# Kernel tuning notes

Hardware: AMD Instinct MI355X
Metric: run time of the kernel (lower is better)

## Reference

```python
import jax, jax.numpy as jnp
import numpy as np

DIS_NORM = 6.0 * 512 / 1000.0  # 6 * D(z=0) * Nmesh / Boxsize with D(0)=1


def setup_inputs() -> dict:
    key = jax.random.key(0)
    x = jax.random.normal(key, (2, 4, 128, 128, 128), dtype=jnp.float32)
    return {"x": x}


def _lag2eul(x):
    N, C = x.shape[0], x.shape[1]
    D, H, W = x.shape[2], x.shape[3], x.shape[4]
    P = D * H * W
    Cout = C - 3 if C > 3 else 1

    # rm_dis_mean=True: mean displacement, detached
    dis_mean = jax.lax.stop_gradient(jnp.mean(x[:, :3], axis=(2, 3, 4), keepdims=True))

    pos = (x[:, :3] - dis_mean) * DIS_NORM  # (N,3,D,H,W)
    gd = jnp.arange(D, dtype=x.dtype) + 0.5
    gh = jnp.arange(H, dtype=x.dtype) + 0.5
    gw = jnp.arange(W, dtype=x.dtype) + 0.5
    grid = jnp.stack(jnp.meshgrid(gd, gh, gw, indexing='ij'))  # (3,D,H,W)
    pos = (pos + grid[None]).reshape(N, 3, P)

    if C > 3:
        val = x[:, 3:].reshape(N, Cout, P)
    else:
        val = jnp.ones((N, Cout, P), dtype=x.dtype)

    intpos = jnp.floor(pos).astype(jnp.int32)
    # 8 trilinear neighbors: bit b of n -> offset along dim b
    neighbors = (jnp.arange(8, dtype=jnp.int32)[None, :] >> jnp.arange(3, dtype=jnp.int32)[:, None]) & 1  # (3,8)
    tgt = intpos[:, :, :, None] + neighbors[None, :, None, :]  # (N,3,P,8)

    kernel = jnp.prod(1.0 - jnp.abs(pos[:, :, :, None] - tgt.astype(x.dtype)), axis=1)  # (N,P,8)
    src = val[:, :, :, None] * kernel[:, None, :, :]  # (N,Cout,P,8)

    # periodic=False: mask out-of-bounds deposits
    bounds = jnp.array([D, H, W], dtype=jnp.int32)[None, :, None, None]
    mask = jnp.all((tgt >= 0) & (tgt < bounds), axis=1)  # (N,P,8)
    ind = (tgt[:, 0] * H + tgt[:, 1]) * W + tgt[:, 2]  # (N,P,8)
    ind = jnp.clip(ind, 0, P - 1)
    src = jnp.where(mask[:, None, :, :], src, jnp.zeros((), dtype=x.dtype))

    def scatter_one(ind_n, src_n):
        mesh = jnp.zeros((Cout, P), dtype=src_n.dtype)
        return mesh.at[:, ind_n.reshape(-1)].add(src_n.reshape(Cout, -1))

    mesh = jax.vmap(scatter_one)(ind, src)  # (N,Cout,P)
    return mesh.reshape(N, Cout, D, H, W)


def reference(x):
    return _lag2eul(x)
```

## Files before the change

kernel.cpp:

```cpp
#include <hip/hip_runtime.h>

#define NBATCH 2
#define NDIM   128
#define NP     (128 * 128 * 128)
#define DIS_NORM 3.072f

#define TS   16
#define LO   5
#define HI   6
#define WIN  (TS + LO + HI)
#define WIN2 (WIN * WIN)
#define WINF (WIN * WIN * WIN)
#define TPB  8
#define NTILE (TPB * TPB * TPB)
#define NTHR 512

#define FXSCALE 16777216.0f
#define FXINV   (1.0f / 16777216.0f)

#define QCAP 1280

#define SLAB 19696

#define SUMS_OFF 0
#define SLABS_OFF 1024
#define WS_FLOATS ((size_t)SLABS_OFF + (size_t)NBATCH * NTILE * SLAB)
#define WS_NEEDED_BYTES (WS_FLOATS * sizeof(float))

__device__ __constant__ int BASE27[27] = {
    0,216,792,972,1548,3084,3564,3744,4224,
    4376,4952,6488,6968,8504,12600,13880,14360,15640,
    16040,16220,16700,16852,17332,18612,19012,19164,19564};

__global__ __launch_bounds__(256) void prep_kernel(const float* __restrict__ x,
                                                   float* __restrict__ ws,
                                                   float* __restrict__ out) {
    const int plane = blockIdx.y;
    if (plane < 6) {
        const int n = plane / 3, c = plane % 3;
        const float4* xp = (const float4*)(x + ((size_t)n * 4 + c) * NP);
        float s = 0.0f;
        for (int i = blockIdx.x * 256 + threadIdx.x; i < NP / 4; i += 128 * 256) {
            float4 v = xp[i];
            s += (v.x + v.y) + (v.z + v.w);
        }
        #pragma unroll
        for (int off = 32; off > 0; off >>= 1) s += __shfl_down(s, off, 64);
        __shared__ float wsum[4];
        if ((threadIdx.x & 63) == 0) wsum[threadIdx.x >> 6] = s;
        __syncthreads();
        if (threadIdx.x == 0)
            ws[SUMS_OFF + plane * 128 + blockIdx.x] =
                (wsum[0] + wsum[1]) + (wsum[2] + wsum[3]);
    } else {
        float4* o4 = (float4*)out;
        const float4 z = make_float4(0.f, 0.f, 0.f, 0.f);
        for (int i = blockIdx.x * 256 + threadIdx.x; i < NBATCH * NP / 4; i += 128 * 256)
            o4[i] = z;
    }
}

__device__ __forceinline__ void load_means128(const float* __restrict__ ws, int n,
                                              float& m0, float& m1, float& m2) {
    float s0 = 0.f, s1 = 0.f, s2 = 0.f;
    const float* p0 = ws + SUMS_OFF + (n * 3 + 0) * 128;
    const float* p1 = ws + SUMS_OFF + (n * 3 + 1) * 128;
    const float* p2 = ws + SUMS_OFF + (n * 3 + 2) * 128;
    #pragma unroll 4
    for (int b = 0; b < 128; ++b) { s0 += p0[b]; s1 += p1[b]; s2 += p2[b]; }
    const float inv_np = 1.0f / (float)NP;
    m0 = s0 * inv_np; m1 = s1 * inv_np; m2 = s2 * inv_np;
}

__device__ __forceinline__ void deposit_pair(unsigned long long* __restrict__ winU,
                                             int b, float va, float vb) {
    const int fa = __float2int_rn(va * FXSCALE);
    const int fb = __float2int_rn(vb * FXSCALE);
    const bool odd = (b & 1);
    const long long packed = (((long long)fb) << 32) + (long long)fa;
    const long long hiOnly = ((long long)fa) << 32;
    atomicAdd(&winU[b >> 1], (unsigned long long)(odd ? hiOnly : packed));
    if (odd) atomicAdd(&winU[(b >> 1) + 1], (unsigned long long)(long long)fb);
}

__device__ __forceinline__ void slow_deposit(unsigned long long* __restrict__ winU,
                                             float* __restrict__ sp,
                                             float pd, float ph, float pw, float v,
                                             int od, int oh, int ow) {
    const float fd = floorf(pd), fh = floorf(ph), fw = floorf(pw);
    const int id = (int)fd, ih = (int)fh, iw = (int)fw;
    const float rd = pd - fd, rh = ph - fh, rw = pw - fw;
    const int wd = id - od, wh = ih - oh, ww = iw - ow;
    const float wd2[2] = {1.0f - rd, rd};
    const float wh2[2] = {1.0f - rh, rh};
    const float ww2[2] = {1.0f - rw, rw};
    #pragma unroll
    for (int dd = 0; dd < 2; ++dd) {
        const int td = id + dd, wdc = wd + dd;
        const bool dW = (unsigned)wdc < WIN, dM = (unsigned)td < NDIM;
        if (!dM && !dW) continue;
        #pragma unroll
        for (int hh = 0; hh < 2; ++hh) {
            const int th = ih + hh, whc = wh + hh;
            const bool hW = (unsigned)whc < WIN, hM = (unsigned)th < NDIM;
            const float vdh = v * wd2[dd] * wh2[hh];
            #pragma unroll
            for (int wi = 0; wi < 2; ++wi) {
                const int tw = iw + wi, wwc = ww + wi;
                const bool wW = (unsigned)wwc < WIN, wM = (unsigned)tw < NDIM;
                const float dep = vdh * ww2[wi];
                if (dW && hW && wW) {
                    const int cb = (wdc * WIN + whc) * WIN + wwc;
                    const int fx = __float2int_rn(dep * FXSCALE);
                    const long long cv = (cb & 1)
                        ? (((long long)fx) << 32) : (long long)fx;
                    atomicAdd(&winU[cb >> 1], (unsigned long long)cv);
                } else if (dM && hM && wM) {
                    atomicAdd(sp + ((size_t)td * NDIM + th) * NDIM + tw, dep);
                }
            }
        }
    }
}

__global__ __launch_bounds__(NTHR, 4) void scatter_tile_kernel(
        const float* __restrict__ x, const float* __restrict__ ws,
        float* __restrict__ slabs, float* __restrict__ out) {
    const int blk = blockIdx.x;
    const int n = blk >> 9;
    const int t = blk & (NTILE - 1);
    const int tx = t & 7, ty = (t >> 3) & 7, tz = t >> 6;

    __shared__ ulonglong2 win2[(WINF + 3) / 4 + 1];
    __shared__ float smean[3];
    __shared__ int qcount;
    __shared__ unsigned short queue[QCAP];
    unsigned long long* winU = (unsigned long long*)win2;
    {
        float4* z4 = (float4*)win2;
        const float4 z = make_float4(0.f, 0.f, 0.f, 0.f);
        for (int i = threadIdx.x; i < (WINF + 3) / 4 + 1; i += NTHR) z4[i] = z;
        if (threadIdx.x == 0) qcount = 0;
    }
    if (threadIdx.x < 192) {
        const int c = threadIdx.x >> 6;
        const int l = threadIdx.x & 63;
        const float* p = ws + SUMS_OFF + (n * 3 + c) * 128;
        float s = p[l] + p[l + 64];
        #pragma unroll
        for (int off = 32; off > 0; off >>= 1) s += __shfl_down(s, off, 64);
        if (l == 0) smean[c] = s * (1.0f / (float)NP);
    }
    __syncthreads();
    const float m0 = smean[0], m1 = smean[1], m2 = smean[2];

    const int i0 = threadIdx.x * 8;
    const int lw0 = i0 & 15;
    const int lh  = (i0 >> 4) & 15;
    const int ld  = i0 >> 8;
    const int gd = tz * TS + ld, gh = ty * TS + lh, gw0 = tx * TS + lw0;
    const size_t prow = ((size_t)gd * NDIM + gh) * NDIM + gw0;

    const float4* x4 = (const float4*)(x + (size_t)n * 4 * NP);
    const size_t q = prow >> 2;
    const size_t s4 = NP / 4;
    float4 a0 = x4[0 * s4 + q], a1 = x4[0 * s4 + q + 1];
    float4 b0 = x4[1 * s4 + q], b1 = x4[1 * s4 + q + 1];
    float4 c0 = x4[2 * s4 + q], c1 = x4[2 * s4 + q + 1];
    float4 e0 = x4[3 * s4 + q], e1 = x4[3 * s4 + q + 1];
    const float D0[8] = {a0.x, a0.y, a0.z, a0.w, a1.x, a1.y, a1.z, a1.w};
    const float D1[8] = {b0.x, b0.y, b0.z, b0.w, b1.x, b1.y, b1.z, b1.w};
    const float D2[8] = {c0.x, c0.y, c0.z, c0.w, c1.x, c1.y, c1.z, c1.w};
    const float VV[8] = {e0.x, e0.y, e0.z, e0.w, e1.x, e1.y, e1.z, e1.w};

    const int od = tz * TS - LO, oh = ty * TS - LO, ow = tx * TS - LO;
    float* sp = out + (size_t)n * NP;

    #pragma unroll
    for (int k = 0; k < 8; ++k) {
        const float pd = (D0[k] - m0) * DIS_NORM + (float)gd + 0.5f;
        const float ph = (D1[k] - m1) * DIS_NORM + (float)gh + 0.5f;
        const float pw = (D2[k] - m2) * DIS_NORM + (float)(gw0 + k) + 0.5f;
        const float v = VV[k];

        const float fd = floorf(pd), fh = floorf(ph), fw = floorf(pw);
        const int id = (int)fd, ih = (int)fh, iw = (int)fw;
        const float rd = pd - fd, rh = ph - fh, rw = pw - fw;

        const int wd = id - od, wh = ih - oh, ww = iw - ow;
        if ((unsigned)wd <= WIN - 2 && (unsigned)wh <= WIN - 2 &&
            (unsigned)ww <= WIN - 2) {
            const int b00 = (wd * WIN + wh) * WIN + ww;
            const float sd0 = v * (1.0f - rd), sd1 = v * rd;
            const float h0 = 1.0f - rh, h1 = rh;
            const float q0 = 1.0f - rw, q1 = rw;
            deposit_pair(winU, b00,              sd0 * h0 * q0, sd0 * h0 * q1);
            deposit_pair(winU, b00 + WIN,        sd0 * h1 * q0, sd0 * h1 * q1);
            deposit_pair(winU, b00 + WIN2,       sd1 * h0 * q0, sd1 * h0 * q1);
            deposit_pair(winU, b00 + WIN2 + WIN, sd1 * h1 * q0, sd1 * h1 * q1);
        } else {
            const int qi = atomicAdd(&qcount, 1);
            if (qi < QCAP) {
                queue[qi] = (unsigned short)(i0 + k);
            } else {
                slow_deposit(winU, sp, pd, ph, pw, v, od, oh, ow);
            }
        }
    }

    __syncthreads();

    {
        const int nq = min(qcount, QCAP);
        const float* xb = x + (size_t)n * 4 * NP;
        for (int qi = threadIdx.x; qi < nq; qi += NTHR) {
            const int p = queue[qi];
            const int lw = p & 15, lhq = (p >> 4) & 15, ldq = p >> 8;
            const int gdq = tz * TS + ldq, ghq = ty * TS + lhq, gwq = tx * TS + lw;
            const size_t pr = ((size_t)gdq * NDIM + ghq) * NDIM + gwq;
            const float pd = (xb[pr] - m0) * DIS_NORM + (float)gdq + 0.5f;
            const float ph = (xb[(size_t)NP + pr] - m1) * DIS_NORM + (float)ghq + 0.5f;
            const float pw = (xb[2 * (size_t)NP + pr] - m2) * DIS_NORM + (float)gwq + 0.5f;
            const float v = xb[3 * (size_t)NP + pr];
            slow_deposit(winU, sp, pd, ph, pw, v, od, oh, ow);
        }
    }
    __syncthreads();

    {
        const int NU = (WINF + 1) / 2;
        for (int i = threadIdx.x; i < NU; i += NTHR) {
            const unsigned long long u = winU[i];
            const int lo = (int)(unsigned)(u & 0xffffffffull);
            const int hi = (int)(u >> 32) + (lo < 0 ? 1 : 0);
            float2 f;
            f.x = (float)lo * FXINV;
            f.y = (float)hi * FXINV;
            ((float2*)winU)[i] = f;
        }
    }
    __syncthreads();
    const float* winF = (const float*)winU;

    const int EXTY[3] = {6, 16, 5};
    const int nbase = n << 9;
    for (int r = threadIdx.x; r < WIN2; r += NTHR) {
        const int lz = r / WIN;
        const int ly = r - lz * WIN;
        int mz, pz;
        if (lz < LO) { mz = -1; pz = lz; }
        else if (lz < LO + TS) { mz = 0; pz = lz - LO; }
        else { mz = 1; pz = lz - LO - TS; }
        int my, py;
        if (ly < LO) { my = -1; py = ly; }
        else if (ly < LO + TS) { my = 0; py = ly - LO; }
        else { my = 1; py = ly - LO - TS; }
        const int dtz = tz + mz, dty = ty + my;
        if ((unsigned)dtz >= TPB || (unsigned)dty >= TPB) continue;

        const int jz = 1 - mz, jy = 1 - my;
        const int ey = EXTY[jy];
        const int rowoff = pz * ey + py;
        const int pobase = jz * 9 + jy * 3;
        const float* src = winF + r * WIN;
        const int slabRow = nbase + (dtz * 8 + dty) * 8;

        if (tx > 0) {
            float* d = slabs + (size_t)(slabRow + tx - 1) * SLAB
                     + BASE27[pobase + 2] + rowoff * 5;
            #pragma unroll
            for (int k = 0; k < 5; ++k) d[k] = src[k];
        }
        {
            float* d = slabs + (size_t)(slabRow + tx) * SLAB
                     + BASE27[pobase + 1] + rowoff * 16;
            #pragma unroll
            for (int k = 0; k < 4; ++k) {
                float4 v;
                v.x = src[5 + 4 * k]; v.y = src[6 + 4 * k];
                v.z = src[7 + 4 * k]; v.w = src[8 + 4 * k];
                ((float4*)d)[k] = v;
            }
        }
        if (tx < TPB - 1) {
            float* d = slabs + (size_t)(slabRow + tx + 1) * SLAB
                     + BASE27[pobase + 0] + rowoff * 6;
            #pragma unroll
            for (int k = 0; k < 6; ++k) d[k] = src[21 + k];
        }
    }
}

__global__ __launch_bounds__(NTHR) void gather_tile_kernel(const float* __restrict__ slabs,
                                                           float* __restrict__ out) {
    const int blk = blockIdx.x;
    const int n = blk >> 9;
    const int t = blk & (NTILE - 1);
    const int tx = t & 7, ty = (t >> 3) & 7, tz = t >> 6;

    const float* __restrict__ slab = slabs + (size_t)blk * SLAB;
    const float4* __restrict__ slab4 = (const float4*)slab;
    float4* __restrict__ o4 = (float4*)(out + (size_t)n * NP);

    for (int i4 = threadIdx.x; i4 < TS * TS * TS / 4; i4 += NTHR) {
        const int xq = i4 & 3, y = (i4 >> 2) & 15, z = i4 >> 6;

        int ysec = 0, yp = 0, ye = 0; bool y2 = false;
        if (y < 6)        { if (ty > 0)       { ysec = 0; yp = y;      ye = 6; y2 = true; } }
        else if (y >= 11) { if (ty < TPB - 1) { ysec = 6; yp = y - 11; ye = 5; y2 = true; } }
        int zsec = 0, zp = 0, ze = 0; bool z2 = false;
        if (z < 6)        { if (tz > 0)       { zsec = 0;  zp = z;      ze = 6; z2 = true; } }
        else if (z >= 11) { if (tz < TPB - 1) { zsec = 18; zp = z - 11; ze = 5; z2 = true; } }

        const int rC = z * 16 + y;
        float4 s = slab4[(BASE27[13] >> 2) + rC * 4 + xq];
        int rY = 0, rZ = 0, rYZ = 0;
        if (y2) {
            rY = z * ye + yp;
            const float4 v = slab4[(BASE27[10 + ysec] >> 2) + rY * 4 + xq];
            s.x += v.x; s.y += v.y; s.z += v.z; s.w += v.w;
        }
        if (z2) {
            rZ = zp * 16 + y;
            const float4 v = slab4[(BASE27[zsec + 4] >> 2) + rZ * 4 + xq];
            s.x += v.x; s.y += v.y; s.z += v.z; s.w += v.w;
            if (y2) {
                rYZ = zp * ye + yp;
                const float4 v2 = slab4[(BASE27[zsec + ysec + 1] >> 2) + rYZ * 4 + xq];
                s.x += v2.x; s.y += v2.y; s.z += v2.z; s.w += v2.w;
            }
        }

        float se[4] = {s.x, s.y, s.z, s.w};
        #pragma unroll
        for (int e = 0; e < 4; ++e) {
            const int x = xq * 4 + e;
            int xsec = 0, xp = 0, xe = 0; bool x2 = false;
            if (x < 6)        { if (tx > 0)       { xsec = 0; xp = x;      xe = 6; x2 = true; } }
            else if (x >= 11) { if (tx < TPB - 1) { xsec = 2; xp = x - 11; xe = 5; x2 = true; } }
            if (x2) {
                se[e] += slab[BASE27[12 + xsec] + rC * xe + xp];
                if (y2) se[e] += slab[BASE27[9 + ysec + xsec] + rY * xe + xp];
                if (z2) {
                    se[e] += slab[BASE27[zsec + 3 + xsec] + rZ * xe + xp];
                    if (y2) se[e] += slab[BASE27[zsec + ysec + xsec] + rYZ * xe + xp];
                }
            }
        }

        const size_t grow = ((size_t)(tz * TS + z) * NDIM + ty * TS + y) * (NDIM / 4)
                          + tx * 4 + xq;
        float4 o = o4[grow];
        o.x += se[0]; o.y += se[1]; o.z += se[2]; o.w += se[3];
        o4[grow] = o;
    }
}

__global__ __launch_bounds__(256) void scatter_direct_kernel(const float* __restrict__ x,
                                                             const float* __restrict__ ws,
                                                             float* __restrict__ out) {
    const int lin = blockIdx.x * 256 + threadIdx.x;
    const int n = lin >> 21;
    const int p = lin & (NP - 1);

    float m0, m1, m2;
    load_means128(ws, n, m0, m1, m2);

    const size_t base = (size_t)n * 4 * NP;
    const float d0 = x[base + 0 * (size_t)NP + p];
    const float d1 = x[base + 1 * (size_t)NP + p];
    const float d2 = x[base + 2 * (size_t)NP + p];
    const float v  = x[base + 3 * (size_t)NP + p];

    const int w = p & 127, h = (p >> 7) & 127, d = p >> 14;
    const float pd = (d0 - m0) * DIS_NORM + (float)d + 0.5f;
    const float ph = (d1 - m1) * DIS_NORM + (float)h + 0.5f;
    const float pw = (d2 - m2) * DIS_NORM + (float)w + 0.5f;
    const float fd = floorf(pd), fh = floorf(ph), fw = floorf(pw);
    const int id = (int)fd, ih = (int)fh, iw = (int)fw;
    const float rd = pd - fd, rh = ph - fh, rw = pw - fw;
    const float wd[2] = {1.0f - rd, rd}, wh[2] = {1.0f - rh, rh}, ww[2] = {1.0f - rw, rw};
    float* o = out + (size_t)n * NP;
    #pragma unroll
    for (int dd = 0; dd < 2; ++dd) {
        const int td = id + dd;
        if ((unsigned)td >= (unsigned)NDIM) continue;
        #pragma unroll
        for (int hh = 0; hh < 2; ++hh) {
            const int th = ih + hh;
            if ((unsigned)th >= (unsigned)NDIM) continue;
            const float vdh = v * wd[dd] * wh[hh];
            const int rowbase = (td * NDIM + th) * NDIM;
            #pragma unroll
            for (int wi = 0; wi < 2; ++wi) {
                const int tw = iw + wi;
                if ((unsigned)tw >= (unsigned)NDIM) continue;
                atomicAdd(o + rowbase + tw, vdh * ww[wi]);
            }
        }
    }
}

extern "C" void kernel_launch(void* const* d_in, const int* in_sizes, int n_in,
                              void* d_out, int out_size, void* d_ws, size_t ws_size,
                              hipStream_t stream) {
    const float* x = (const float*)d_in[0];
    float* out = (float*)d_out;
    float* ws = (float*)d_ws;
    float* slabs = ws + SLABS_OFF;

    dim3 pgrid(128, 7);

    if (ws_size >= WS_NEEDED_BYTES) {
        prep_kernel<<<pgrid, 256, 0, stream>>>(x, ws, out);
        scatter_tile_kernel<<<dim3(NBATCH * NTILE), NTHR, 0, stream>>>(x, ws, slabs, out);
        gather_tile_kernel<<<dim3(NBATCH * NTILE), NTHR, 0, stream>>>(slabs, out);
    } else {
        prep_kernel<<<pgrid, 256, 0, stream>>>(x, ws, out);
        scatter_direct_kernel<<<dim3(NBATCH * NP / 256), 256, 0, stream>>>(x, ws, out);
    }
}
```

Measured before the change: 186.6 us.

## Fuse prep, scatter and gather into one cooperative kernel with grid syncs

Replaces the three-launch pipeline (prep, scatter_tile, gather_tile) with a single cooperative kernel of 512 blocks. Each block zeroes output and computes partial sums, then processes two tiles per phase, with grid.sync separating the phases. This is meant to remove launch gaps and tail effects between kernels, and it shrinks the shared-memory overflow queue to raise occupancy. The cost is grid-wide barriers and fewer blocks each doing twice the work, with a fallback to the old path if a cooperative launch is unavailable.

Measured after the change: 186.4 us. About the same (-0.1%).

```diff
diff --git a/kernel.cpp b/kernel.cpp
--- a/kernel.cpp
+++ b/kernel.cpp
@@ -1,4 +1,7 @@
 #include <hip/hip_runtime.h>
+#include <hip/hip_cooperative_groups.h>
+
+namespace cg = cooperative_groups;
 
 #define NBATCH 2
 #define NDIM   128
@@ -14,11 +17,13 @@
 #define TPB  8
 #define NTILE (TPB * TPB * TPB)
 #define NTHR 512
+#define NBLK 512
 
 #define FXSCALE 16777216.0f
 #define FXINV   (1.0f / 16777216.0f)
 
-#define QCAP 1280
+#define QCAP_F 384
+#define QCAP   1280
 
 #define SLAB 19696
 
@@ -31,46 +36,6 @@
     0,216,792,972,1548,3084,3564,3744,4224,
     4376,4952,6488,6968,8504,12600,13880,14360,15640,
     16040,16220,16700,16852,17332,18612,19012,19164,19564};
-
-__global__ __launch_bounds__(256) void prep_kernel(const float* __restrict__ x,
-                                                   float* __restrict__ ws,
-                                                   float* __restrict__ out) {
-    const int plane = blockIdx.y;
-    if (plane < 6) {
-        const int n = plane / 3, c = plane % 3;
-        const float4* xp = (const float4*)(x + ((size_t)n * 4 + c) * NP);
-        float s = 0.0f;
-        for (int i = blockIdx.x * 256 + threadIdx.x; i < NP / 4; i += 128 * 256) {
-            float4 v = xp[i];
-            s += (v.x + v.y) + (v.z + v.w);
-        }
-        #pragma unroll
-        for (int off = 32; off > 0; off >>= 1) s += __shfl_down(s, off, 64);
-        __shared__ float wsum[4];
-        if ((threadIdx.x & 63) == 0) wsum[threadIdx.x >> 6] = s;
-        __syncthreads();
-        if (threadIdx.x == 0)
-            ws[SUMS_OFF + plane * 128 + blockIdx.x] =
-                (wsum[0] + wsum[1]) + (wsum[2] + wsum[3]);
-    } else {
-        float4* o4 = (float4*)out;
-        const float4 z = make_float4(0.f, 0.f, 0.f, 0.f);
-        for (int i = blockIdx.x * 256 + threadIdx.x; i < NBATCH * NP / 4; i += 128 * 256)
-            o4[i] = z;
-    }
-}
-
-__device__ __forceinline__ void load_means128(const float* __restrict__ ws, int n,
-                                              float& m0, float& m1, float& m2) {
-    float s0 = 0.f, s1 = 0.f, s2 = 0.f;
-    const float* p0 = ws + SUMS_OFF + (n * 3 + 0) * 128;
-    const float* p1 = ws + SUMS_OFF + (n * 3 + 1) * 128;
-    const float* p2 = ws + SUMS_OFF + (n * 3 + 2) * 128;
-    #pragma unroll 4
-    for (int b = 0; b < 128; ++b) { s0 += p0[b]; s1 += p1[b]; s2 += p2[b]; }
-    const float inv_np = 1.0f / (float)NP;
-    m0 = s0 * inv_np; m1 = s1 * inv_np; m2 = s2 * inv_np;
-}
 
 __device__ __forceinline__ void deposit_pair(unsigned long long* __restrict__ winU,
                                              int b, float va, float vb) {
@@ -123,6 +88,312 @@
     }
 }
 
+__global__ __launch_bounds__(NTHR, 4) void fused_kernel(const float* __restrict__ x,
+                                                        float* __restrict__ ws,
+                                                        float* __restrict__ out) {
+    cg::grid_group grid = cg::this_grid();
+    const int b = blockIdx.x;
+    const int tid = threadIdx.x;
+
+    __shared__ ulonglong2 win2[(WINF + 3) / 4 + 1];
+    __shared__ float smean[3];
+    __shared__ float wsum8[8];
+    __shared__ int qcount;
+    __shared__ unsigned short queue[QCAP_F];
+    unsigned long long* winU = (unsigned long long*)win2;
+
+    {
+        float4* o4 = (float4*)out;
+        const float4 z = make_float4(0.f, 0.f, 0.f, 0.f);
+        for (int i = b * NTHR + tid; i < NBATCH * NP / 4; i += NBLK * NTHR)
+            o4[i] = z;
+    }
+    if (b < 384) {
+        const int plane = b >> 6, chunk = b & 63;
+        const float4* xp = (const float4*)(x + ((size_t)(plane / 3) * 4 + plane % 3) * NP);
+        float s = 0.0f;
+        for (int i = chunk * NTHR + tid; i < NP / 4; i += 64 * NTHR) {
+            float4 v = xp[i];
+            s += (v.x + v.y) + (v.z + v.w);
+        }
+        #pragma unroll
+        for (int off = 32; off > 0; off >>= 1) s += __shfl_down(s, off, 64);
+        if ((tid & 63) == 0) wsum8[tid >> 6] = s;
+        __syncthreads();
+        if (tid == 0) {
+            float t = 0.f;
+            #pragma unroll
+            for (int w = 0; w < 8; ++w) t += wsum8[w];
+            ws[SUMS_OFF + plane * 64 + chunk] = t;
+        }
+    }
+    grid.sync();
+
+    float* slabs = ws + SLABS_OFF;
+    for (int rep = 0; rep < 2; ++rep) {
+        const int blk = b + rep * NBLK;
+        const int n = blk >> 9;
+        const int t = blk & (NTILE - 1);
+        const int tx = t & 7, ty = (t >> 3) & 7, tz = t >> 6;
+
+        __syncthreads();
+        {
+            float4* z4 = (float4*)win2;
+            const float4 z = make_float4(0.f, 0.f, 0.f, 0.f);
+            for (int i = tid; i < (WINF + 3) / 4 + 1; i += NTHR) z4[i] = z;
+            if (tid == 0) qcount = 0;
+        }
+        if (tid < 192) {
+            const int c = tid >> 6;
+            const int l = tid & 63;
+            float s = ws[SUMS_OFF + (n * 3 + c) * 64 + l];
+            #pragma unroll
+            for (int off = 32; off > 0; off >>= 1) s += __shfl_down(s, off, 64);
+            if (l == 0) smean[c] = s * (1.0f / (float)NP);
+        }
+        __syncthreads();
+        const float m0 = smean[0], m1 = smean[1], m2 = smean[2];
+
+        const int i0 = tid * 8;
+        const int lw0 = i0 & 15;
+        const int lh  = (i0 >> 4) & 15;
+        const int ld  = i0 >> 8;
+        const int gd = tz * TS + ld, gh = ty * TS + lh, gw0 = tx * TS + lw0;
+        const size_t prow = ((size_t)gd * NDIM + gh) * NDIM + gw0;
+
+        const float4* x4 = (const float4*)(x + (size_t)n * 4 * NP);
+        const size_t q = prow >> 2;
+        const size_t s4 = NP / 4;
+        float4 a0 = x4[0 * s4 + q], a1 = x4[0 * s4 + q + 1];
+        float4 b0 = x4[1 * s4 + q], b1 = x4[1 * s4 + q + 1];
+        float4 c0 = x4[2 * s4 + q], c1 = x4[2 * s4 + q + 1];
+        float4 e0 = x4[3 * s4 + q], e1 = x4[3 * s4 + q + 1];
+        const float D0[8] = {a0.x, a0.y, a0.z, a0.w, a1.x, a1.y, a1.z, a1.w};
+        const float D1[8] = {b0.x, b0.y, b0.z, b0.w, b1.x, b1.y, b1.z, b1.w};
+        const float D2[8] = {c0.x, c0.y, c0.z, c0.w, c1.x, c1.y, c1.z, c1.w};
+        const float VV[8] = {e0.x, e0.y, e0.z, e0.w, e1.x, e1.y, e1.z, e1.w};
+
+        const int od = tz * TS - LO, oh = ty * TS - LO, ow = tx * TS - LO;
+        float* sp = out + (size_t)n * NP;
+
+        #pragma unroll
+        for (int k = 0; k < 8; ++k) {
+            const float pd = (D0[k] - m0) * DIS_NORM + (float)gd + 0.5f;
+            const float ph = (D1[k] - m1) * DIS_NORM + (float)gh + 0.5f;
+            const float pw = (D2[k] - m2) * DIS_NORM + (float)(gw0 + k) + 0.5f;
+            const float v = VV[k];
+
+            const float fd = floorf(pd), fh = floorf(ph), fw = floorf(pw);
+            const int id = (int)fd, ih = (int)fh, iw = (int)fw;
+            const float rd = pd - fd, rh = ph - fh, rw = pw - fw;
+
+            const int wd = id - od, wh = ih - oh, ww = iw - ow;
+            if ((unsigned)wd <= WIN - 2 && (unsigned)wh <= WIN - 2 &&
+                (unsigned)ww <= WIN - 2) {
+                const int b00 = (wd * WIN + wh) * WIN + ww;
+                const float sd0 = v * (1.0f - rd), sd1 = v * rd;
+                const float h0 = 1.0f - rh, h1 = rh;
+                const float q0 = 1.0f - rw, q1 = rw;
+                deposit_pair(winU, b00,              sd0 * h0 * q0, sd0 * h0 * q1);
+                deposit_pair(winU, b00 + WIN,        sd0 * h1 * q0, sd0 * h1 * q1);
+                deposit_pair(winU, b00 + WIN2,       sd1 * h0 * q0, sd1 * h0 * q1);
+                deposit_pair(winU, b00 + WIN2 + WIN, sd1 * h1 * q0, sd1 * h1 * q1);
+            } else {
+                const int qi = atomicAdd(&qcount, 1);
+                if (qi < QCAP_F) queue[qi] = (unsigned short)(i0 + k);
+                else slow_deposit(winU, sp, pd, ph, pw, v, od, oh, ow);
+            }
+        }
+
+        __syncthreads();
+
+        {
+            const int nq = min(qcount, QCAP_F);
+            const float* xb = x + (size_t)n * 4 * NP;
+            for (int qi = tid; qi < nq; qi += NTHR) {
+                const int p = queue[qi];
+                const int lw = p & 15, lhq = (p >> 4) & 15, ldq = p >> 8;
+                const int gdq = tz * TS + ldq, ghq = ty * TS + lhq, gwq = tx * TS + lw;
+                const size_t pr = ((size_t)gdq * NDIM + ghq) * NDIM + gwq;
+                const float pd = (xb[pr] - m0) * DIS_NORM + (float)gdq + 0.5f;
+                const float ph = (xb[(size_t)NP + pr] - m1) * DIS_NORM + (float)ghq + 0.5f;
+                const float pw = (xb[2 * (size_t)NP + pr] - m2) * DIS_NORM + (float)gwq + 0.5f;
+                const float v = xb[3 * (size_t)NP + pr];
+                slow_deposit(winU, sp, pd, ph, pw, v, od, oh, ow);
+            }
+        }
+        __syncthreads();
+
+        {
+            const int NU = (WINF + 1) / 2;
+            for (int i = tid; i < NU; i += NTHR) {
+                const unsigned long long u = winU[i];
+                const int lo = (int)(unsigned)(u & 0xffffffffull);
+                const int hi = (int)(u >> 32) + (lo < 0 ? 1 : 0);
+                float2 f;
+                f.x = (float)lo * FXINV;
+                f.y = (float)hi * FXINV;
+                ((float2*)winU)[i] = f;
+            }
+        }
+        __syncthreads();
+        const float* winF = (const float*)winU;
+
+        const int EXTY[3] = {6, 16, 5};
+        const int nbase = n << 9;
+        for (int r = tid; r < WIN2; r += NTHR) {
+            const int lz = r / WIN;
+            const int ly = r - lz * WIN;
+            int mz, pz;
+            if (lz < LO) { mz = -1; pz = lz; }
+            else if (lz < LO + TS) { mz = 0; pz = lz - LO; }
+            else { mz = 1; pz = lz - LO - TS; }
+            int my, py;
+            if (ly < LO) { my = -1; py = ly; }
+            else if (ly < LO + TS) { my = 0; py = ly - LO; }
+            else { my = 1; py = ly - LO - TS; }
+            const int dtz = tz + mz, dty = ty + my;
+            if ((unsigned)dtz >= TPB || (unsigned)dty >= TPB) continue;
+
+            const int jz = 1 - mz, jy = 1 - my;
+            const int ey = EXTY[jy];
+            const int rowoff = pz * ey + py;
+            const int pobase = jz * 9 + jy * 3;
+            const float* src = winF + r * WIN;
+            const int slabRow = nbase + (dtz * 8 + dty) * 8;
+
+            if (tx > 0) {
+                float* d = slabs + (size_t)(slabRow + tx - 1) * SLAB
+                         + BASE27[pobase + 2] + rowoff * 5;
+                #pragma unroll
+                for (int k = 0; k < 5; ++k) d[k] = src[k];
+            }
+            {
+                float* d = slabs + (size_t)(slabRow + tx) * SLAB
+                         + BASE27[pobase + 1] + rowoff * 16;
+                #pragma unroll
+                for (int k = 0; k < 4; ++k) {
+                    float4 v;
+                    v.x = src[5 + 4 * k]; v.y = src[6 + 4 * k];
+                    v.z = src[7 + 4 * k]; v.w = src[8 + 4 * k];
+                    ((float4*)d)[k] = v;
+                }
+            }
+            if (tx < TPB - 1) {
+                float* d = slabs + (size_t)(slabRow + tx + 1) * SLAB
+                         + BASE27[pobase + 0] + rowoff * 6;
+                #pragma unroll
+                for (int k = 0; k < 6; ++k) d[k] = src[21 + k];
+            }
+        }
+    }
+    grid.sync();
+
+    for (int rep = 0; rep < 2; ++rep) {
+        const int blk = b + rep * NBLK;
+        const int n = blk >> 9;
+        const int t = blk & (NTILE - 1);
+        const int tx = t & 7, ty = (t >> 3) & 7, tz = t >> 6;
+
+        const float* __restrict__ slab = slabs + (size_t)blk * SLAB;
+        const float4* __restrict__ slab4 = (const float4*)slab;
+        float4* __restrict__ o4 = (float4*)(out + (size_t)n * NP);
+
+        for (int i4 = tid; i4 < TS * TS * TS / 4; i4 += NTHR) {
+            const int xq = i4 & 3, y = (i4 >> 2) & 15, z = i4 >> 6;
+
+            int ysec = 0, yp = 0, ye = 0; bool y2 = false;
+            if (y < 6)        { if (ty > 0)       { ysec = 0; yp = y;      ye = 6; y2 = true; } }
+            else if (y >= 11) { if (ty < TPB - 1) { ysec = 6; yp = y - 11; ye = 5; y2 = true; } }
+            int zsec = 0, zp = 0; bool z2 = false;
+            if (z < 6)        { if (tz > 0)       { zsec = 0;  zp = z;      z2 = true; } }
+            else if (z >= 11) { if (tz < TPB - 1) { zsec = 18; zp = z - 11; z2 = true; } }
+
+            const int rC = z * 16 + y;
+            float4 s = slab4[(BASE27[13] >> 2) + rC * 4 + xq];
+            int rY = 0, rZ = 0, rYZ = 0;
+            if (y2) {
+                rY = z * ye + yp;
+                const float4 v = slab4[(BASE27[10 + ysec] >> 2) + rY * 4 + xq];
+                s.x += v.x; s.y += v.y; s.z += v.z; s.w += v.w;
+            }
+            if (z2) {
+                rZ = zp * 16 + y;
+                const float4 v = slab4[(BASE27[zsec + 4] >> 2) + rZ * 4 + xq];
+                s.x += v.x; s.y += v.y; s.z += v.z; s.w += v.w;
+                if (y2) {
+                    rYZ = zp * ye + yp;
+                    const float4 v2 = slab4[(BASE27[zsec + ysec + 1] >> 2) + rYZ * 4 + xq];
+                    s.x += v2.x; s.y += v2.y; s.z += v2.z; s.w += v2.w;
+                }
+            }
+
+            float se[4] = {s.x, s.y, s.z, s.w};
+            #pragma unroll
+            for (int e = 0; e < 4; ++e) {
+                const int xx = xq * 4 + e;
+                int xsec = 0, xp = 0, xe = 0; bool x2 = false;
+                if (xx < 6)        { if (tx > 0)       { xsec = 0; xp = xx;      xe = 6; x2 = true; } }
+                else if (xx >= 11) { if (tx < TPB - 1) { xsec = 2; xp = xx - 11; xe = 5; x2 = true; } }
+                if (x2) {
+                    se[e] += slab[BASE27[12 + xsec] + rC * xe + xp];
+                    if (y2) se[e] += slab[BASE27[9 + ysec + xsec] + rY * xe + xp];
+                    if (z2) {
+                        se[e] += slab[BASE27[zsec + 3 + xsec] + rZ * xe + xp];
+                        if (y2) se[e] += slab[BASE27[zsec + ysec + xsec] + rYZ * xe + xp];
+                    }
+                }
+            }
+
+            const size_t grow = ((size_t)(tz * TS + z) * NDIM + ty * TS + y) * (NDIM / 4)
+                              + tx * 4 + xq;
+            float4 o = o4[grow];
+            o.x += se[0]; o.y += se[1]; o.z += se[2]; o.w += se[3];
+            o4[grow] = o;
+        }
+    }
+}
+
+__global__ __launch_bounds__(256) void prep_kernel(const float* __restrict__ x,
+                                                   float* __restrict__ ws,
+                                                   float* __restrict__ out) {
+    const int plane = blockIdx.y;
+    if (plane < 6) {
+        const int n = plane / 3, c = plane % 3;
+        const float4* xp = (const float4*)(x + ((size_t)n * 4 + c) * NP);
+        float s = 0.0f;
+        for (int i = blockIdx.x * 256 + threadIdx.x; i < NP / 4; i += 128 * 256) {
+            float4 v = xp[i];
+            s += (v.x + v.y) + (v.z + v.w);
+        }
+        #pragma unroll
+        for (int off = 32; off > 0; off >>= 1) s += __shfl_down(s, off, 64);
+        __shared__ float wsum[4];
+        if ((threadIdx.x & 63) == 0) wsum[threadIdx.x >> 6] = s;
+        __syncthreads();
+        if (threadIdx.x == 0)
+            ws[SUMS_OFF + plane * 128 + blockIdx.x] =
+                (wsum[0] + wsum[1]) + (wsum[2] + wsum[3]);
+    } else {
+        float4* o4 = (float4*)out;
+        const float4 z = make_float4(0.f, 0.f, 0.f, 0.f);
+        for (int i = blockIdx.x * 256 + threadIdx.x; i < NBATCH * NP / 4; i += 128 * 256)
+            o4[i] = z;
+    }
+}
+
+__device__ __forceinline__ void load_means128(const float* __restrict__ ws, int n,
+                                              float& m0, float& m1, float& m2) {
+    float s0 = 0.f, s1 = 0.f, s2 = 0.f;
+    const float* p0 = ws + SUMS_OFF + (n * 3 + 0) * 128;
+    const float* p1 = ws + SUMS_OFF + (n * 3 + 1) * 128;
+    const float* p2 = ws + SUMS_OFF + (n * 3 + 2) * 128;
+    #pragma unroll 4
+    for (int b = 0; b < 128; ++b) { s0 += p0[b]; s1 += p1[b]; s2 += p2[b]; }
+    const float inv_np = 1.0f / (float)NP;
+    m0 = s0 * inv_np; m1 = s1 * inv_np; m2 = s2 * inv_np;
+}
+
 __global__ __launch_bounds__(NTHR, 4) void scatter_tile_kernel(
         const float* __restrict__ x, const float* __restrict__ ws,
         float* __restrict__ slabs, float* __restrict__ out) {
@@ -200,11 +471,8 @@
             deposit_pair(winU, b00 + WIN2 + WIN, sd1 * h1 * q0, sd1 * h1 * q1);
         } else {
             const int qi = atomicAdd(&qcount, 1);
-            if (qi < QCAP) {
-                queue[qi] = (unsigned short)(i0 + k);
-            } else {
-                slow_deposit(winU, sp, pd, ph, pw, v, od, oh, ow);
-            }
+            if (qi < QCAP) queue[qi] = (unsigned short)(i0 + k);
+            else slow_deposit(winU, sp, pd, ph, pw, v, od, oh, ow);
         }
     }
 
@@ -308,9 +576,9 @@
         int ysec = 0, yp = 0, ye = 0; bool y2 = false;
         if (y < 6)        { if (ty > 0)       { ysec = 0; yp = y;      ye = 6; y2 = true; } }
         else if (y >= 11) { if (ty < TPB - 1) { ysec = 6; yp = y - 11; ye = 5; y2 = true; } }
-        int zsec = 0, zp = 0, ze = 0; bool z2 = false;
-        if (z < 6)        { if (tz > 0)       { zsec = 0;  zp = z;      ze = 6; z2 = true; } }
-        else if (z >= 11) { if (tz < TPB - 1) { zsec = 18; zp = z - 11; ze = 5; z2 = true; } }
+        int zsec = 0, zp = 0; bool z2 = false;
+        if (z < 6)        { if (tz > 0)       { zsec = 0;  zp = z;      z2 = true; } }
+        else if (z >= 11) { if (tz < TPB - 1) { zsec = 18; zp = z - 11; z2 = true; } }
 
         const int rC = z * 16 + y;
         float4 s = slab4[(BASE27[13] >> 2) + rC * 4 + xq];
@@ -334,10 +602,10 @@
         float se[4] = {s.x, s.y, s.z, s.w};
         #pragma unroll
         for (int e = 0; e < 4; ++e) {
-            const int x = xq * 4 + e;
+            const int xx = xq * 4 + e;
             int xsec = 0, xp = 0, xe = 0; bool x2 = false;
-            if (x < 6)        { if (tx > 0)       { xsec = 0; xp = x;      xe = 6; x2 = true; } }
-            else if (x >= 11) { if (tx < TPB - 1) { xsec = 2; xp = x - 11; xe = 5; x2 = true; } }
+            if (xx < 6)        { if (tx > 0)       { xsec = 0; xp = xx;      xe = 6; x2 = true; } }
+            else if (xx >= 11) { if (tx < TPB - 1) { xsec = 2; xp = xx - 11; xe = 5; x2 = true; } }
             if (x2) {
                 se[e] += slab[BASE27[12 + xsec] + rC * xe + xp];
                 if (y2) se[e] += slab[BASE27[9 + ysec + xsec] + rY * xe + xp];
@@ -401,6 +669,8 @@
     }
 }
 
+static int g_coop_state = -1;
+
 extern "C" void kernel_launch(void* const* d_in, const int* in_sizes, int n_in,
                               void* d_out, int out_size, void* d_ws, size_t ws_size,
                               hipStream_t stream) {
@@ -409,13 +679,33 @@
     float* ws = (float*)d_ws;
     float* slabs = ws + SLABS_OFF;
 
-    dim3 pgrid(128, 7);
+    if (g_coop_state < 0) {
+        int dev = 0;
+        (void)hipGetDevice(&dev);
+        int coop = 0;
+        (void)hipDeviceGetAttribute(&coop, hipDeviceAttributeCooperativeLaunch, dev);
+        int occ = 0;
+        hipError_t oe = hipOccupancyMaxActiveBlocksPerMultiprocessor(
+            &occ, (const void*)fused_kernel, NTHR, 0);
+        g_coop_state = (coop != 0 && oe == hipSuccess && occ >= 2) ? 1 : 0;
+    }
+
+    if (ws_size >= WS_NEEDED_BYTES && g_coop_state == 1) {
+        void* args[] = {(void*)&x, (void*)&ws, (void*)&out};
+        hipError_t err = hipLaunchCooperativeKernel((const void*)fused_kernel,
+                                                    dim3(NBLK), dim3(NTHR),
+                                                    args, 0, stream);
+        if (err == hipSuccess) return;
+        g_coop_state = 0;
+    }
 
     if (ws_size >= WS_NEEDED_BYTES) {
+        dim3 pgrid(128, 7);
         prep_kernel<<<pgrid, 256, 0, stream>>>(x, ws, out);
         scatter_tile_kernel<<<dim3(NBATCH * NTILE), NTHR, 0, stream>>>(x, ws, slabs, out);
         gather_tile_kernel<<<dim3(NBATCH * NTILE), NTHR, 0, stream>>>(slabs, out);
     } else {
+        dim3 pgrid(128, 7);
         prep_kernel<<<pgrid, 256, 0, stream>>>(x, ws, out);
         scatter_direct_kernel<<<dim3(NBATCH * NP / 256), 256, 0, stream>>>(x, ws, out);
     }
```
